# Performance work log

Hardware: AMD Instinct MI355X
Metric: run time of the kernel (lower is better)

Reference implementation:

```python
import jax, jax.numpy as jnp
import numpy as np

TAU = 0.2
LW = 0.5
EPS = 1e-12  # tf.math.l2_normalize epsilon


def _l2norm(x):
    ss = jnp.sum(x * x, axis=-1, keepdims=True)
    return x * jax.lax.rsqrt(jnp.maximum(ss, EPS))


def _global_head(f, W1, b1, W2, b2):
    g = jnp.mean(f, axis=(1, 2))            # GlobalAveragePooling2D -> [B, C]
    h = jax.nn.relu(g @ W1 + b1)
    return h @ W2 + b2                      # [B, 128]


def _dense_head(f, W1, b1, W2, b2):
    # 1x1 convs == per-pixel matmuls
    h = jax.nn.relu(jnp.einsum('bhwc,cd->bhwd', f, W1) + b1)
    return jnp.einsum('bhwd,de->bhwe', h, W2) + b2  # [B, H, W, 128]


def _info_nce(q, k):
    logits = (q @ k.T) / TAU                # [N, N]
    lse = jax.nn.logsumexp(logits, axis=-1)
    pos = jnp.diagonal(logits)
    return jnp.mean(lse - pos)


def setup_inputs() -> dict:
    key = jax.random.key(0)
    ks = jax.random.split(key, 10)
    B, H, W, C = 128, 7, 7, 2048
    Dh, De = 2048, 128
    s1 = 1.0 / np.sqrt(C)
    s2 = 1.0 / np.sqrt(Dh)
    inp = {
        'feat_q': jax.random.normal(ks[0], (B, H, W, C), jnp.float32),
        'feat_k': jax.random.normal(ks[1], (B, H, W, C), jnp.float32),
        'Wg1': jax.random.normal(ks[2], (C, Dh), jnp.float32) * s1,
        'bg1': jnp.zeros((Dh,), jnp.float32),
        'Wg2': jax.random.normal(ks[3], (Dh, De), jnp.float32) * s2,
        'bg2': jnp.zeros((De,), jnp.float32),
        'Wd1': jax.random.normal(ks[4], (C, Dh), jnp.float32) * s1,
        'bd1': jnp.zeros((Dh,), jnp.float32),
        'Wd2': jax.random.normal(ks[5], (Dh, De), jnp.float32) * s2,
        'bd2': jnp.zeros((De,), jnp.float32),
        'mWg1': jax.random.normal(ks[6], (C, Dh), jnp.float32) * s1,
        'mbg1': jnp.zeros((Dh,), jnp.float32),
        'mWg2': jax.random.normal(ks[7], (Dh, De), jnp.float32) * s2,
        'mbg2': jnp.zeros((De,), jnp.float32),
        'mWd1': jax.random.normal(ks[8], (C, Dh), jnp.float32) * s1,
        'mbd1': jnp.zeros((Dh,), jnp.float32),
        'mWd2': jax.random.normal(ks[9], (Dh, De), jnp.float32) * s2,
        'mbd2': jnp.zeros((De,), jnp.float32),
    }
    return inp


def reference(feat_q, feat_k, Wg1, bg1, Wg2, bg2, Wd1, bd1, Wd2, bd2,
              mWg1, mbg1, mWg2, mbg2, mWd1, mbd1, mWd2, mbd2):
    # query (student) branch
    q_g = _l2norm(_global_head(feat_q, Wg1, bg1, Wg2, bg2))      # [B, 128]
    q_d = _l2norm(_dense_head(feat_q, Wd1, bd1, Wd2, bd2))       # [B, H, W, 128]
    # key (momentum teacher) branch, stop-gradient as in train_step
    k_g = jax.lax.stop_gradient(_l2norm(_global_head(feat_k, mWg1, mbg1, mWg2, mbg2)))
    k_d = jax.lax.stop_gradient(_l2norm(_dense_head(feat_k, mWd1, mbd1, mWd2, mbd2)))

    l_g = _info_nce(q_g, k_g)

    B, H, W, De = q_d.shape
    f1 = q_d.reshape(B, H * W, De)
    f2 = k_d.reshape(B, H * W, De)
    sim = jnp.einsum('bnc,bmc->bnm', f1, f2)                     # [B, HW, HW]
    idx = jnp.argmax(sim, axis=-1)                               # [B, HW]
    matched = jnp.take_along_axis(f2, idx[..., None], axis=1)    # [B, HW, 128]

    l_d = _info_nce(f1.reshape(-1, De), matched.reshape(-1, De))
    total = (1.0 - LW) * l_g + LW * l_d
    return total
```

## Files before the change

kernel.cpp:

```cpp
#include <hip/hip_runtime.h>
#include <cstddef>

typedef __bf16 bf16x8 __attribute__((ext_vector_type(8)));
typedef float  f32x4  __attribute__((ext_vector_type(4)));
typedef unsigned short u16x8 __attribute__((ext_vector_type(8)));

__device__ __forceinline__ float b2f(unsigned short u) {
    union { unsigned int i; float f; } v; v.i = ((unsigned int)u) << 16; return v.f;
}
__device__ __forceinline__ unsigned short f2b(float f) {
    union { float f; unsigned int i; } v; v.f = f;
    unsigned int r = v.i + 0x7fffu + ((v.i >> 16) & 1u);
    return (unsigned short)(r >> 16);
}
__device__ __forceinline__ void gl_lds16(const void* g, void* l) {
    __builtin_amdgcn_global_load_lds((const __attribute__((address_space(1))) void*)g,
                                     (__attribute__((address_space(3))) void*)l,
                                     16, 0, 0);
}

__global__ __launch_bounds__(64) void detect_kernel(const unsigned short* __restrict__ feat,
                                                    int* __restrict__ flag) {
    __shared__ int cnt;
    if (threadIdx.x == 0) cnt = 0;
    __syncthreads();
    int c = 0;
    for (int i = threadIdx.x; i < 256; i += 64) {
        float v = b2f(feat[i]);
        if (fabsf(v) > 100.0f) ++c;
    }
    atomicAdd(&cnt, c);
    __syncthreads();
    if (threadIdx.x == 0) *flag = (cnt > 16) ? 1 : 0;
}

__global__ __launch_bounds__(256) void zero_kernel(float* __restrict__ p, int n4) {
    int i = blockIdx.x * 256 + threadIdx.x;
    const f32x4 z = {0.f, 0.f, 0.f, 0.f};
    if (i < n4) ((f32x4*)p)[i] = z;
}

__global__ __launch_bounds__(256) void pool_kernel(const void* __restrict__ fq,
                                                   const void* __restrict__ fk,
                                                   unsigned short* __restrict__ gq,
                                                   unsigned short* __restrict__ gk,
                                                   const int* __restrict__ flagp) {
    int fl = *flagp;
    int c = blockIdx.x * 256 + threadIdx.x;
    int b = blockIdx.y;
    const void* src = blockIdx.z ? fk : fq;
    unsigned short* dst = blockIdx.z ? gk : gq;
    size_t base = (size_t)b * 49 * 2048 + c;
    float s = 0.f;
    if (fl) {
        const float* sf = (const float*)src;
        #pragma unroll
        for (int p = 0; p < 49; ++p) s += sf[base + (size_t)p * 2048];
    } else {
        const unsigned short* su = (const unsigned short*)src;
        #pragma unroll
        for (int p = 0; p < 49; ++p) s += b2f(su[base + (size_t)p * 2048]);
    }
    dst[(size_t)b * 2048 + c] = f2b(s * (1.0f / 49.0f));
}

__global__ __launch_bounds__(256) void transpose4v_kernel(
    const void* __restrict__ s0, const void* __restrict__ s1,
    const void* __restrict__ s2, const void* __restrict__ s3,
    unsigned short* __restrict__ d0, unsigned short* __restrict__ d1,
    unsigned short* __restrict__ d2, unsigned short* __restrict__ d3,
    int rows, int cols, const int* __restrict__ flagp) {
    int fl = *flagp;
    int z = blockIdx.z;
    const void* in = (z == 0) ? s0 : (z == 1) ? s1 : (z == 2) ? s2 : s3;
    unsigned short* out = (z == 0) ? d0 : (z == 1) ? d1 : (z == 2) ? d2 : d3;
    __shared__ unsigned short tile[64 * 72];
    int bx = blockIdx.x * 64, by = blockIdx.y * 64;
    int tr = threadIdx.x >> 3;
    int tc = (threadIdx.x & 7) * 8;
    #pragma unroll
    for (int h = 0; h < 2; ++h) {
        int r = tr + h * 32;
        if (fl) {
            const float* inf = (const float*)in + (size_t)(by + r) * cols + bx + tc;
            f32x4 v0 = *(const f32x4*)inf;
            f32x4 v1 = *(const f32x4*)(inf + 4);
            u16x8 o;
            o[0]=f2b(v0[0]); o[1]=f2b(v0[1]); o[2]=f2b(v0[2]); o[3]=f2b(v0[3]);
            o[4]=f2b(v1[0]); o[5]=f2b(v1[1]); o[6]=f2b(v1[2]); o[7]=f2b(v1[3]);
            *(u16x8*)(tile + r * 72 + tc) = o;
        } else {
            const unsigned short* inu = (const unsigned short*)in + (size_t)(by + r) * cols + bx + tc;
            *(u16x8*)(tile + r * 72 + tc) = *(const u16x8*)inu;
        }
    }
    __syncthreads();
    #pragma unroll
    for (int h = 0; h < 2; ++h) {
        int oc = tr + h * 32;
        u16x8 v;
        #pragma unroll
        for (int j = 0; j < 8; ++j) v[j] = tile[(tc + j) * 72 + oc];
        *(u16x8*)(out + (size_t)(bx + oc) * rows + by + tc) = v;
    }
}

__global__ __launch_bounds__(256) void mlp_kernel(
    const void* __restrict__ Aq, const void* __restrict__ Ak,
    const unsigned short* __restrict__ gq, const unsigned short* __restrict__ gk,
    const unsigned short* __restrict__ BTdq, const unsigned short* __restrict__ BTdk,
    const unsigned short* __restrict__ BTgq, const unsigned short* __restrict__ BTgk,
    const unsigned short* __restrict__ W2dq, const unsigned short* __restrict__ W2dk,
    const unsigned short* __restrict__ W2gq, const unsigned short* __restrict__ W2gk,
    const void* __restrict__ b1dq, const void* __restrict__ b1dk,
    const void* __restrict__ b1gq, const void* __restrict__ b1gk,
    float* __restrict__ outdq, float* __restrict__ outdk,
    float* __restrict__ outgq, float* __restrict__ outgk,
    const int* __restrict__ flagp)
{
    int fl = *flagp;
    int z  = blockIdx.z;
    int isg = (blockIdx.y == 49);
    const void* A; const unsigned short* Bt; const unsigned short* W2;
    const void* b1; float* outp;
    if (!isg) {
        A = z ? Ak : Aq;  Bt = z ? BTdk : BTdq;  W2 = z ? W2dk : W2dq;
        b1 = z ? b1dk : b1dq;  outp = z ? outdk : outdq;
    } else {
        A = z ? (const void*)gk : (const void*)gq;  Bt = z ? BTgk : BTgq;
        W2 = z ? W2gk : W2gq;  b1 = z ? b1gk : b1gq;  outp = z ? outgk : outgq;
    }
    int af32 = (!isg) && fl;
    const int K = 2048;

    __shared__ unsigned short smem[8192 + 9216];
    unsigned short* As = smem;
    unsigned short* Bs = smem + 8192;
    unsigned short* Hs = smem + 8192;

    int tid  = threadIdx.x;
    int lane = tid & 63;
    int w    = tid >> 6;
    int wm = w & 1, wn = w >> 1;
    int quad = lane >> 4, l16 = lane & 15;
    size_t m0 = isg ? 0 : (size_t)blockIdx.y * 128;
    size_t n0 = (size_t)blockIdx.x * 128;

    int lrow = lane >> 3;
    int kc   = (lane & 7) ^ lrow;

    const unsigned short* gA[4];
    const unsigned short* gB[4];
    unsigned short* lA[4];
    unsigned short* lB[4];
    if (!af32) {
        const unsigned short* Au = (const unsigned short*)A;
        #pragma unroll
        for (int c = 0; c < 4; ++c) {
            int row = w * 32 + c * 8 + lrow;
            gA[c] = Au + (m0 + row) * (size_t)K + kc * 8;
            lA[c] = As + w * 2048 + c * 512;
        }
    }
    #pragma unroll
    for (int c = 0; c < 4; ++c) {
        int row = w * 32 + c * 8 + lrow;
        gB[c] = Bt + (n0 + row) * (size_t)K + kc * 8;
        lB[c] = Bs + w * 2048 + c * 512;
    }

    const f32x4 zero4 = {0.f, 0.f, 0.f, 0.f};
    f32x4 acc[4][4];
    #pragma unroll
    for (int i = 0; i < 4; ++i)
        #pragma unroll
        for (int j = 0; j < 4; ++j) acc[i][j] = zero4;

    int swz = l16 & 7;
    for (int kb = 0; kb < K / 64; ++kb) {
        __syncthreads();
        if (af32) {
            const float* Af = (const float*)A;
            #pragma unroll
            for (int i = 0; i < 4; ++i) {
                int l = tid + 256 * i;
                int row = l >> 3, kcp = l & 7;
                int kcg = kcp ^ (row & 7);
                size_t gidx = (m0 + row) * (size_t)K + kb * 64 + kcg * 8;
                f32x4 v0 = *(const f32x4*)(Af + gidx);
                f32x4 v1 = *(const f32x4*)(Af + gidx + 4);
                u16x8 o;
                o[0]=f2b(v0[0]); o[1]=f2b(v0[1]); o[2]=f2b(v0[2]); o[3]=f2b(v0[3]);
                o[4]=f2b(v1[0]); o[5]=f2b(v1[1]); o[6]=f2b(v1[2]); o[7]=f2b(v1[3]);
                *(u16x8*)(As + row * 64 + kcp * 8) = o;
            }
        } else {
            #pragma unroll
            for (int c = 0; c < 4; ++c) { gl_lds16(gA[c], lA[c]); gA[c] += 64; }
        }
        #pragma unroll
        for (int c = 0; c < 4; ++c) { gl_lds16(gB[c], lB[c]); gB[c] += 64; }
        __syncthreads();
        #pragma unroll
        for (int k0 = 0; k0 < 64; k0 += 32) {
            bf16x8 af[4], bfr[4];
            #pragma unroll
            for (int mt = 0; mt < 4; ++mt) {
                int row = wm * 64 + mt * 16 + l16;
                int sc  = (((k0 >> 3) + quad) ^ swz) << 3;
                af[mt] = *(const bf16x8*)(As + row * 64 + sc);
            }
            #pragma unroll
            for (int nt = 0; nt < 4; ++nt) {
                int row = wn * 64 + nt * 16 + l16;
                int sc  = (((k0 >> 3) + quad) ^ swz) << 3;
                bfr[nt] = *(const bf16x8*)(Bs + row * 64 + sc);
            }
            #pragma unroll
            for (int mt = 0; mt < 4; ++mt)
                #pragma unroll
                for (int nt = 0; nt < 4; ++nt)
                    acc[mt][nt] = __builtin_amdgcn_mfma_f32_16x16x32_bf16(af[mt], bfr[nt], acc[mt][nt], 0, 0, 0);
        }
    }

    float b1v[4];
    #pragma unroll
    for (int nt = 0; nt < 4; ++nt) {
        int col = (int)n0 + wn * 64 + nt * 16 + l16;
        b1v[nt] = fl ? ((const float*)b1)[col] : b2f(((const unsigned short*)b1)[col]);
    }

    f32x4 acc2[4][4];
    #pragma unroll
    for (int i = 0; i < 4; ++i)
        #pragma unroll
        for (int j = 0; j < 4; ++j) acc2[i][j] = zero4;

    #pragma unroll
    for (int hf = 0; hf < 2; ++hf) {
        __syncthreads();
        if (wn == hf) {
            #pragma unroll
            for (int mt = 0; mt < 4; ++mt)
                #pragma unroll
                for (int nt = 0; nt < 4; ++nt)
                    #pragma unroll
                    for (int r = 0; r < 4; ++r) {
                        float v = fmaxf(acc[mt][nt][r] + b1v[nt], 0.f);
                        Hs[(wm * 64 + mt * 16 + quad * 4 + r) * 72 + nt * 16 + l16] = f2b(v);
                    }
        } else {
            #pragma unroll
            for (int c = 0; c < 8; ++c) {
                const unsigned short* g = W2 + (size_t)(wm * 64 + c * 8 + lrow) * 2048
                                          + n0 + hf * 64 + kc * 8;
                gl_lds16(g, As + wm * 4096 + c * 512);
            }
        }
        __syncthreads();
        #pragma unroll
        for (int k0 = 0; k0 < 64; k0 += 32) {
            bf16x8 ha[4], wb[4];
            #pragma unroll
            for (int mt = 0; mt < 4; ++mt)
                ha[mt] = *(const bf16x8*)(Hs + (wm * 64 + mt * 16 + l16) * 72 + k0 + quad * 8);
            #pragma unroll
            for (int et = 0; et < 4; ++et) {
                int row = wn * 64 + et * 16 + l16;
                int sc  = (((k0 >> 3) + quad) ^ swz) << 3;
                wb[et] = *(const bf16x8*)(As + row * 64 + sc);
            }
            #pragma unroll
            for (int mt = 0; mt < 4; ++mt)
                #pragma unroll
                for (int et = 0; et < 4; ++et)
                    acc2[mt][et] = __builtin_amdgcn_mfma_f32_16x16x32_bf16(ha[mt], wb[et], acc2[mt][et], 0, 0, 0);
        }
    }

    #pragma unroll
    for (int et = 0; et < 4; ++et) {
        int col = wn * 64 + et * 16 + l16;
        #pragma unroll
        for (int mt = 0; mt < 4; ++mt)
            #pragma unroll
            for (int r = 0; r < 4; ++r) {
                size_t row = m0 + wm * 64 + mt * 16 + quad * 4 + r;
                atomicAdd(&outp[row * 128 + col], acc2[mt][et][r]);
            }
    }
}

__global__ __launch_bounds__(256) void simmatch_kernel(
    const float* __restrict__ rawdq, const float* __restrict__ rawdk,
    const void* __restrict__ bd2, const void* __restrict__ mbd2,
    unsigned short* __restrict__ qd, unsigned short* __restrict__ kd,
    unsigned short* __restrict__ matched, float* __restrict__ pos,
    const int* __restrict__ flagp) {
    int fl = *flagp;
    __shared__ float f1s[49 * 128];
    __shared__ float f2s[49 * 128];
    int b = blockIdx.x;
    int t = threadIdx.x;
    size_t base = (size_t)b * 49 * 128;

    int rr = t >> 2, jq = t & 3;
    if (rr < 49) {
        #pragma unroll
        for (int br = 0; br < 2; ++br) {
            const float* raw = br ? rawdk : rawdq;
            const void* bias = br ? mbd2 : bd2;
            unsigned short* outg = br ? kd : qd;
            float* fs = br ? f2s : f1s;
            size_t idx = base + (size_t)rr * 128 + jq * 32;
            float x[32];
            float ss = 0.f;
            #pragma unroll
            for (int c = 0; c < 32; ++c) {
                float bv = fl ? ((const float*)bias)[jq * 32 + c]
                              : b2f(((const unsigned short*)bias)[jq * 32 + c]);
                x[c] = raw[idx + c] + bv;
                ss += x[c] * x[c];
            }
            ss += __shfl_xor(ss, 1); ss += __shfl_xor(ss, 2);
            float rs = rsqrtf(fmaxf(ss, 1e-12f));
            #pragma unroll
            for (int c = 0; c < 32; ++c) {
                unsigned short us = f2b(x[c] * rs);
                outg[idx + c] = us;
                fs[rr * 128 + jq * 32 + c] = b2f(us);
            }
        }
    }
    __syncthreads();

    int i = t >> 2, q4 = t & 3;
    if (i < 49) {
        int mlo = q4 * 13;
        int mhi = mlo + 13; if (mhi > 49) mhi = 49;
        float best = -1e30f; int bi = 1 << 20;
        const f32x4* va = (const f32x4*)(f1s + i * 128);
        for (int m = mlo; m < mhi; ++m) {
            const f32x4* vb = (const f32x4*)(f2s + m * 128);
            float d = 0.f;
            #pragma unroll
            for (int j = 0; j < 32; ++j) {
                f32x4 a = va[j], bb = vb[j];
                d += a[0]*bb[0] + a[1]*bb[1] + a[2]*bb[2] + a[3]*bb[3];
            }
            if (d > best) { best = d; bi = m; }
        }
        #pragma unroll
        for (int off = 1; off < 4; off <<= 1) {
            float ov = __shfl_xor(best, off);
            int   oi = __shfl_xor(bi, off);
            if (ov > best || (ov == best && oi < bi)) { best = ov; bi = oi; }
        }
        if (q4 == 0) pos[b * 49 + i] = best * 5.0f;
        for (int j = q4 * 32; j < q4 * 32 + 32; ++j)
            matched[base + (size_t)i * 128 + j] = f2b(f2s[bi * 128 + j]);
    }
}

#define KS 136
__global__ __launch_bounds__(256) void lse_kernel(const unsigned short* __restrict__ qd,
                                                  const unsigned short* __restrict__ matched,
                                                  float* __restrict__ lsep) {
    __shared__ unsigned short As[128 * KS];
    __shared__ unsigned short Bs[64 * KS];
    __shared__ float rsum[128];
    int tid  = threadIdx.x;
    int lane = tid & 63, wave = tid >> 6;
    int wm = wave & 1, wn = wave >> 1;
    int quad = lane >> 4, l16 = lane & 15;
    size_t m0 = (size_t)blockIdx.x * 128;
    int z = blockIdx.y;

    #pragma unroll
    for (int i = 0; i < 8; ++i) {
        int l = tid + 256 * i;
        int row = l >> 4, ko = (l & 15) << 3;
        u16x8 v = *(const u16x8*)(qd + (m0 + row) * 128 + ko);
        *(u16x8*)(As + row * KS + ko) = v;
    }
    if (tid < 128) rsum[tid] = 0.f;

    float rs[4][4];
    #pragma unroll
    for (int mt = 0; mt < 4; ++mt)
        #pragma unroll
        for (int r = 0; r < 4; ++r) rs[mt][r] = 0.f;

    const f32x4 zero4 = {0.f, 0.f, 0.f, 0.f};
    int nlo = z * 448, nhi = nlo + 448;
    for (int n0 = nlo; n0 < nhi; n0 += 64) {
        __syncthreads();
        #pragma unroll
        for (int i = 0; i < 4; ++i) {
            int l = tid + 256 * i;
            int row = l >> 4, ko = (l & 15) << 3;
            u16x8 v = *(const u16x8*)(matched + (size_t)(n0 + row) * 128 + ko);
            *(u16x8*)(Bs + row * KS + ko) = v;
        }
        __syncthreads();
        f32x4 acc[4][2];
        #pragma unroll
        for (int mt = 0; mt < 4; ++mt) { acc[mt][0] = zero4; acc[mt][1] = zero4; }
        #pragma unroll
        for (int k0 = 0; k0 < 128; k0 += 32) {
            bf16x8 af[4], bfr[2];
            #pragma unroll
            for (int mt = 0; mt < 4; ++mt)
                af[mt] = *(const bf16x8*)(As + (wm * 64 + mt * 16 + l16) * KS + k0 + quad * 8);
            #pragma unroll
            for (int nt = 0; nt < 2; ++nt)
                bfr[nt] = *(const bf16x8*)(Bs + (wn * 32 + nt * 16 + l16) * KS + k0 + quad * 8);
            #pragma unroll
            for (int mt = 0; mt < 4; ++mt)
                #pragma unroll
                for (int nt = 0; nt < 2; ++nt)
                    acc[mt][nt] = __builtin_amdgcn_mfma_f32_16x16x32_bf16(af[mt], bfr[nt], acc[mt][nt], 0, 0, 0);
        }
        #pragma unroll
        for (int mt = 0; mt < 4; ++mt)
            #pragma unroll
            for (int r = 0; r < 4; ++r)
                rs[mt][r] += __expf(acc[mt][0][r] * 5.0f) + __expf(acc[mt][1][r] * 5.0f);
    }
    #pragma unroll
    for (int mt = 0; mt < 4; ++mt)
        #pragma unroll
        for (int r = 0; r < 4; ++r) {
            float v = rs[mt][r];
            v += __shfl_xor(v, 1); v += __shfl_xor(v, 2);
            v += __shfl_xor(v, 4); v += __shfl_xor(v, 8);
            if (l16 == 0) atomicAdd(&rsum[wm * 64 + mt * 16 + quad * 4 + r], v);
        }
    __syncthreads();
    if (tid < 128) lsep[(size_t)z * 6272 + m0 + tid] = rsum[tid];
}

__global__ __launch_bounds__(128) void lg_kernel(const float* __restrict__ rawgq,
                                                 const float* __restrict__ rawgk,
                                                 const void* __restrict__ bg2,
                                                 const void* __restrict__ mbg2,
                                                 float* __restrict__ lgrow,
                                                 const int* __restrict__ flagp) {
    int fl = *flagp;
    __shared__ float ksf[128 * 128];
    __shared__ float qsf[8 * 128];
    int t = threadIdx.x;
    int rbase = blockIdx.x * 8;
    {
        const float* rk = rawgk + (size_t)t * 128;
        float ss = 0.f;
        for (int c = 0; c < 128; ++c) {
            float bv = fl ? ((const float*)mbg2)[c] : b2f(((const unsigned short*)mbg2)[c]);
            float xx = rk[c] + bv;
            ss += xx * xx;
        }
        float rsv = rsqrtf(fmaxf(ss, 1e-12f));
        for (int c = 0; c < 128; ++c) {
            float bv = fl ? ((const float*)mbg2)[c] : b2f(((const unsigned short*)mbg2)[c]);
            ksf[t * 128 + c] = b2f(f2b((rk[c] + bv) * rsv));
        }
    }
    if (t < 8) {
        const float* rq = rawgq + (size_t)(rbase + t) * 128;
        float ss = 0.f;
        for (int c = 0; c < 128; ++c) {
            float bv = fl ? ((const float*)bg2)[c] : b2f(((const unsigned short*)bg2)[c]);
            float xx = rq[c] + bv;
            ss += xx * xx;
        }
        float rsv = rsqrtf(fmaxf(ss, 1e-12f));
        for (int c = 0; c < 128; ++c) {
            float bv = fl ? ((const float*)bg2)[c] : b2f(((const unsigned short*)bg2)[c]);
            qsf[t * 128 + c] = b2f(f2b((rq[c] + bv) * rsv));
        }
    }
    __syncthreads();
    int rl = t >> 4, jg = t & 15;
    int row = rbase + rl;
    float se = 0.f, diag = 0.f;
    for (int jj = 0; jj < 8; ++jj) {
        int j = jg * 8 + jj;
        float d = 0.f;
        #pragma unroll 8
        for (int c = 0; c < 128; ++c) d += qsf[rl * 128 + c] * ksf[j * 128 + c];
        d *= 5.0f;
        se += __expf(d);
        if (j == row) diag = d;
    }
    #pragma unroll
    for (int off = 1; off < 16; off <<= 1) { se += __shfl_xor(se, off); diag += __shfl_xor(diag, off); }
    if (jg == 0) lgrow[row] = logf(se) - diag;
}

__global__ __launch_bounds__(256) void final_kernel(const float* __restrict__ lsep,
                                                    const float* __restrict__ pos,
                                                    const float* __restrict__ lgrow,
                                                    unsigned int* __restrict__ out) {
    int t = threadIdx.x;
    float s = 0.f;
    for (int i = t; i < 6272; i += 256) {
        float se = 0.f;
        #pragma unroll
        for (int zz = 0; zz < 14; ++zz) se += lsep[zz * 6272 + i];
        s += logf(se) - pos[i];
    }
    float g = (t < 128) ? lgrow[t] : 0.f;
    #pragma unroll
    for (int off = 32; off >= 1; off >>= 1) { s += __shfl_xor(s, off); g += __shfl_xor(g, off); }
    __shared__ float p8[8];
    if ((t & 63) == 0) { p8[t >> 6] = s; p8[4 + (t >> 6)] = g; }
    __syncthreads();
    if (t == 0) {
        float ld  = (p8[0] + p8[1] + p8[2] + p8[3]) * (1.0f / 6272.0f);
        float lg  = (p8[4] + p8[5] + p8[6] + p8[7]) * (1.0f / 128.0f);
        float total = 0.5f * lg + 0.5f * ld;
        unsigned int L = f2b(total);
        union { float f; unsigned int u; } tb; tb.f = total;
        unsigned int base = (tb.u & 0xFFFF0000u) | L;
        unsigned int bu = base; float be = 1e30f;
        #pragma unroll
        for (int d = -1; d <= 1; ++d) {
            unsigned int c = base + ((unsigned int)d << 16);
            union { unsigned int u; float f; } cv; cv.u = c;
            float e = fabsf(cv.f - total);
            if (e < be) { be = e; bu = c; }
        }
        out[0] = bu;
    }
}

#define BT1Q_OFF  ((size_t)0)
#define QD_OFF    ((size_t)0)
#define KD_OFF    ((size_t)1605632)
#define MT_OFF    ((size_t)3211264)
#define BT1K_OFF  ((size_t)8388608)
#define BTGQ_OFF  ((size_t)16777216)
#define BTGK_OFF  ((size_t)25165824)
#define W2DQ_OFF  ((size_t)33554432)
#define W2DK_OFF  ((size_t)34078720)
#define W2GQ_OFF  ((size_t)34603008)
#define W2GK_OFF  ((size_t)35127296)
#define RAWDQ_OFF ((size_t)35651584)
#define RAWDK_OFF ((size_t)38862848)
#define RAWGQ_OFF ((size_t)42074112)
#define RAWGK_OFF ((size_t)42139648)
#define GQ_OFF    ((size_t)42205184)
#define GK_OFF    ((size_t)42729472)
#define POS_OFF   ((size_t)43253760)
#define LSEP_OFF  ((size_t)43278848)
#define LGR_OFF   ((size_t)43630080)
#define FLAG_OFF  ((size_t)43630592)

extern "C" void kernel_launch(void* const* d_in, const int* in_sizes, int n_in,
                              void* d_out, int out_size, void* d_ws, size_t ws_size,
                              hipStream_t stream) {
    (void)in_sizes; (void)n_in; (void)out_size; (void)ws_size;
    const void* feat_q = d_in[0];
    const void* feat_k = d_in[1];
    const void* Wg1 = d_in[2];  const void* bg1 = d_in[3];
    const void* Wg2 = d_in[4];  const void* bg2 = d_in[5];
    const void* Wd1 = d_in[6];  const void* bd1 = d_in[7];
    const void* Wd2 = d_in[8];  const void* bd2 = d_in[9];
    const void* mWg1 = d_in[10]; const void* mbg1 = d_in[11];
    const void* mWg2 = d_in[12]; const void* mbg2 = d_in[13];
    const void* mWd1 = d_in[14]; const void* mbd1 = d_in[15];
    const void* mWd2 = d_in[16]; const void* mbd2 = d_in[17];

    char* ws = (char*)d_ws;
    unsigned short* BT1q = (unsigned short*)(ws + BT1Q_OFF);
    unsigned short* BT1k = (unsigned short*)(ws + BT1K_OFF);
    unsigned short* BTgq = (unsigned short*)(ws + BTGQ_OFF);
    unsigned short* BTgk = (unsigned short*)(ws + BTGK_OFF);
    unsigned short* W2dq = (unsigned short*)(ws + W2DQ_OFF);
    unsigned short* W2dk = (unsigned short*)(ws + W2DK_OFF);
    unsigned short* W2gq = (unsigned short*)(ws + W2GQ_OFF);
    unsigned short* W2gk = (unsigned short*)(ws + W2GK_OFF);
    float* rawdq = (float*)(ws + RAWDQ_OFF);
    float* rawdk = (float*)(ws + RAWDK_OFF);
    float* rawgq = (float*)(ws + RAWGQ_OFF);
    float* rawgk = (float*)(ws + RAWGK_OFF);
    unsigned short* gq = (unsigned short*)(ws + GQ_OFF);
    unsigned short* gk = (unsigned short*)(ws + GK_OFF);
    unsigned short* qd = (unsigned short*)(ws + QD_OFF);
    unsigned short* kd = (unsigned short*)(ws + KD_OFF);
    unsigned short* mt = (unsigned short*)(ws + MT_OFF);
    float* pos  = (float*)(ws + POS_OFF);
    float* lsep = (float*)(ws + LSEP_OFF);
    float* lgr  = (float*)(ws + LGR_OFF);
    int*   flag = (int*)(ws + FLAG_OFF);

    detect_kernel<<<1, 64, 0, stream>>>((const unsigned short*)feat_q, flag);

    transpose4v_kernel<<<dim3(32, 32, 4), 256, 0, stream>>>(
        Wd1, mWd1, Wg1, mWg1, BT1q, BT1k, BTgq, BTgk, 2048, 2048, flag);
    transpose4v_kernel<<<dim3(2, 32, 4), 256, 0, stream>>>(
        Wd2, mWd2, Wg2, mWg2, W2dq, W2dk, W2gq, W2gk, 2048, 128, flag);

    pool_kernel<<<dim3(8, 128, 2), 256, 0, stream>>>(feat_q, feat_k, gq, gk, flag);

    zero_kernel<<<1600, 256, 0, stream>>>(rawdq, 409600);

    mlp_kernel<<<dim3(16, 50, 2), 256, 0, stream>>>(
        feat_q, feat_k, gq, gk,
        BT1q, BT1k, BTgq, BTgk,
        W2dq, W2dk, W2gq, W2gk,
        bd1, mbd1, bg1, mbg1,
        rawdq, rawdk, rawgq, rawgk, flag);

    simmatch_kernel<<<128, 256, 0, stream>>>(rawdq, rawdk, bd2, mbd2, qd, kd, mt, pos, flag);
    lse_kernel<<<dim3(49, 14), 256, 0, stream>>>(qd, mt, lsep);
    lg_kernel<<<16, 128, 0, stream>>>(rawgq, rawgk, bg2, mbg2, lgr, flag);
    final_kernel<<<1, 256, 0, stream>>>(lsep, pos, lgr, (unsigned int*)d_out);
}
```

Measured before the change: 641.4 us.

## Pre-convert features to bf16 and split MLP into sequential passes with reused buffers

Fp32 features are converted to bf16 in a separate pass, so the MLP GEMM always uses direct global-to-LDS loads instead of converting inline. The single fused launch covering global and dense, query and key, becomes sequential launches that reuse two workspace slots, which shrinks the working set and may improve L2 residency. The LSE split count drops from 14 to 7 to halve partial results. The cost is more launches, an extra read and write of each feature tensor, and less parallelism per launch.

```diff
diff --git a/kernel.cpp b/kernel.cpp
--- a/kernel.cpp
+++ b/kernel.cpp
@@ -38,6 +38,24 @@
     int i = blockIdx.x * 256 + threadIdx.x;
     const f32x4 z = {0.f, 0.f, 0.f, 0.f};
     if (i < n4) ((f32x4*)p)[i] = z;
+}
+
+__global__ __launch_bounds__(256) void convert_kernel(const void* __restrict__ in,
+                                                      unsigned short* __restrict__ out,
+                                                      const int* __restrict__ flagp) {
+    int fl = *flagp;
+    size_t i = ((size_t)blockIdx.x * 256 + threadIdx.x) * 8;
+    if (fl) {
+        const float* inf = (const float*)in;
+        f32x4 v0 = *(const f32x4*)(inf + i);
+        f32x4 v1 = *(const f32x4*)(inf + i + 4);
+        u16x8 o;
+        o[0]=f2b(v0[0]); o[1]=f2b(v0[1]); o[2]=f2b(v0[2]); o[3]=f2b(v0[3]);
+        o[4]=f2b(v1[0]); o[5]=f2b(v1[1]); o[6]=f2b(v1[2]); o[7]=f2b(v1[3]);
+        *(u16x8*)(out + i) = o;
+    } else {
+        *(u16x8*)(out + i) = *(const u16x8*)((const unsigned short*)in + i);
+    }
 }
 
 __global__ __launch_bounds__(256) void pool_kernel(const void* __restrict__ fq,
@@ -64,6 +82,45 @@
     dst[(size_t)b * 2048 + c] = f2b(s * (1.0f / 49.0f));
 }
 
+__global__ __launch_bounds__(256) void transpose2v_kernel(
+    const void* __restrict__ s0, const void* __restrict__ s1,
+    unsigned short* __restrict__ d0, unsigned short* __restrict__ d1,
+    int rows, int cols, const int* __restrict__ flagp) {
+    int fl = *flagp;
+    int z = blockIdx.z;
+    const void* in = z ? s1 : s0;
+    unsigned short* out = z ? d1 : d0;
+    __shared__ unsigned short tile[64 * 72];
+    int bx = blockIdx.x * 64, by = blockIdx.y * 64;
+    int tr = threadIdx.x >> 3;
+    int tc = (threadIdx.x & 7) * 8;
+    #pragma unroll
+    for (int h = 0; h < 2; ++h) {
+        int r = tr + h * 32;
+        if (fl) {
+            const float* inf = (const float*)in + (size_t)(by + r) * cols + bx + tc;
+            f32x4 v0 = *(const f32x4*)inf;
+            f32x4 v1 = *(const f32x4*)(inf + 4);
+            u16x8 o;
+            o[0]=f2b(v0[0]); o[1]=f2b(v0[1]); o[2]=f2b(v0[2]); o[3]=f2b(v0[3]);
+            o[4]=f2b(v1[0]); o[5]=f2b(v1[1]); o[6]=f2b(v1[2]); o[7]=f2b(v1[3]);
+            *(u16x8*)(tile + r * 72 + tc) = o;
+        } else {
+            const unsigned short* inu = (const unsigned short*)in + (size_t)(by + r) * cols + bx + tc;
+            *(u16x8*)(tile + r * 72 + tc) = *(const u16x8*)inu;
+        }
+    }
+    __syncthreads();
+    #pragma unroll
+    for (int h = 0; h < 2; ++h) {
+        int oc = tr + h * 32;
+        u16x8 v;
+        #pragma unroll
+        for (int j = 0; j < 8; ++j) v[j] = tile[(tc + j) * 72 + oc];
+        *(u16x8*)(out + (size_t)(bx + oc) * rows + by + tc) = v;
+    }
+}
+
 __global__ __launch_bounds__(256) void transpose4v_kernel(
     const void* __restrict__ s0, const void* __restrict__ s1,
     const void* __restrict__ s2, const void* __restrict__ s3,
@@ -106,31 +163,20 @@
 }
 
 __global__ __launch_bounds__(256) void mlp_kernel(
-    const void* __restrict__ Aq, const void* __restrict__ Ak,
-    const unsigned short* __restrict__ gq, const unsigned short* __restrict__ gk,
-    const unsigned short* __restrict__ BTdq, const unsigned short* __restrict__ BTdk,
-    const unsigned short* __restrict__ BTgq, const unsigned short* __restrict__ BTgk,
-    const unsigned short* __restrict__ W2dq, const unsigned short* __restrict__ W2dk,
-    const unsigned short* __restrict__ W2gq, const unsigned short* __restrict__ W2gk,
-    const void* __restrict__ b1dq, const void* __restrict__ b1dk,
-    const void* __restrict__ b1gq, const void* __restrict__ b1gk,
-    float* __restrict__ outdq, float* __restrict__ outdk,
-    float* __restrict__ outgq, float* __restrict__ outgk,
+    const unsigned short* __restrict__ A0, const unsigned short* __restrict__ A1,
+    const unsigned short* __restrict__ Bt0, const unsigned short* __restrict__ Bt1,
+    const unsigned short* __restrict__ W20, const unsigned short* __restrict__ W21,
+    const void* __restrict__ b10, const void* __restrict__ b11,
+    float* __restrict__ out0, float* __restrict__ out1,
     const int* __restrict__ flagp)
 {
     int fl = *flagp;
     int z  = blockIdx.z;
-    int isg = (blockIdx.y == 49);
-    const void* A; const unsigned short* Bt; const unsigned short* W2;
-    const void* b1; float* outp;
-    if (!isg) {
-        A = z ? Ak : Aq;  Bt = z ? BTdk : BTdq;  W2 = z ? W2dk : W2dq;
-        b1 = z ? b1dk : b1dq;  outp = z ? outdk : outdq;
-    } else {
-        A = z ? (const void*)gk : (const void*)gq;  Bt = z ? BTgk : BTgq;
-        W2 = z ? W2gk : W2gq;  b1 = z ? b1gk : b1gq;  outp = z ? outgk : outgq;
-    }
-    int af32 = (!isg) && fl;
+    const unsigned short* A  = z ? A1 : A0;
+    const unsigned short* Bt = z ? Bt1 : Bt0;
+    const unsigned short* W2 = z ? W21 : W20;
+    const void* b1 = z ? b11 : b10;
+    float* outp = z ? out1 : out0;
     const int K = 2048;
 
     __shared__ unsigned short smem[8192 + 9216];
@@ -143,7 +189,7 @@
     int w    = tid >> 6;
     int wm = w & 1, wn = w >> 1;
     int quad = lane >> 4, l16 = lane & 15;
-    size_t m0 = isg ? 0 : (size_t)blockIdx.y * 128;
+    size_t m0 = (size_t)blockIdx.y * 128;
     size_t n0 = (size_t)blockIdx.x * 128;
 
     int lrow = lane >> 3;
@@ -153,19 +199,12 @@
     const unsigned short* gB[4];
     unsigned short* lA[4];
     unsigned short* lB[4];
-    if (!af32) {
-        const unsigned short* Au = (const unsigned short*)A;
-        #pragma unroll
-        for (int c = 0; c < 4; ++c) {
-            int row = w * 32 + c * 8 + lrow;
-            gA[c] = Au + (m0 + row) * (size_t)K + kc * 8;
-            lA[c] = As + w * 2048 + c * 512;
-        }
-    }
     #pragma unroll
     for (int c = 0; c < 4; ++c) {
         int row = w * 32 + c * 8 + lrow;
+        gA[c] = A  + (m0 + row) * (size_t)K + kc * 8;
         gB[c] = Bt + (n0 + row) * (size_t)K + kc * 8;
+        lA[c] = As + w * 2048 + c * 512;
         lB[c] = Bs + w * 2048 + c * 512;
     }
 
@@ -179,25 +218,8 @@
     int swz = l16 & 7;
     for (int kb = 0; kb < K / 64; ++kb) {
         __syncthreads();
-        if (af32) {
-            const float* Af = (const float*)A;
-            #pragma unroll
-            for (int i = 0; i < 4; ++i) {
-                int l = tid + 256 * i;
-                int row = l >> 3, kcp = l & 7;
-                int kcg = kcp ^ (row & 7);
-                size_t gidx = (m0 + row) * (size_t)K + kb * 64 + kcg * 8;
-                f32x4 v0 = *(const f32x4*)(Af + gidx);
-                f32x4 v1 = *(const f32x4*)(Af + gidx + 4);
-                u16x8 o;
-                o[0]=f2b(v0[0]); o[1]=f2b(v0[1]); o[2]=f2b(v0[2]); o[3]=f2b(v0[3]);
-                o[4]=f2b(v1[0]); o[5]=f2b(v1[1]); o[6]=f2b(v1[2]); o[7]=f2b(v1[3]);
-                *(u16x8*)(As + row * 64 + kcp * 8) = o;
-            }
-        } else {
-            #pragma unroll
-            for (int c = 0; c < 4; ++c) { gl_lds16(gA[c], lA[c]); gA[c] += 64; }
-        }
+        #pragma unroll
+        for (int c = 0; c < 4; ++c) { gl_lds16(gA[c], lA[c]); gA[c] += 64; }
         #pragma unroll
         for (int c = 0; c < 4; ++c) { gl_lds16(gB[c], lB[c]); gB[c] += 64; }
         __syncthreads();
@@ -393,7 +415,7 @@
         for (int r = 0; r < 4; ++r) rs[mt][r] = 0.f;
 
     const f32x4 zero4 = {0.f, 0.f, 0.f, 0.f};
-    int nlo = z * 448, nhi = nlo + 448;
+    int nlo = z * 896, nhi = nlo + 896;
     for (int n0 = nlo; n0 < nhi; n0 += 64) {
         __syncthreads();
         #pragma unroll
@@ -507,7 +529,7 @@
     for (int i = t; i < 6272; i += 256) {
         float se = 0.f;
         #pragma unroll
-        for (int zz = 0; zz < 14; ++zz) se += lsep[zz * 6272 + i];
+        for (int zz = 0; zz < 7; ++zz) se += lsep[zz * 6272 + i];
         s += logf(se) - pos[i];
     }
     float g = (t < 128) ? lgrow[t] : 0.f;
@@ -535,27 +557,25 @@
     }
 }
 
-#define BT1Q_OFF  ((size_t)0)
+#define SLOTA_OFF ((size_t)0)
 #define QD_OFF    ((size_t)0)
 #define KD_OFF    ((size_t)1605632)
 #define MT_OFF    ((size_t)3211264)
-#define BT1K_OFF  ((size_t)8388608)
-#define BTGQ_OFF  ((size_t)16777216)
-#define BTGK_OFF  ((size_t)25165824)
-#define W2DQ_OFF  ((size_t)33554432)
-#define W2DK_OFF  ((size_t)34078720)
-#define W2GQ_OFF  ((size_t)34603008)
-#define W2GK_OFF  ((size_t)35127296)
-#define RAWDQ_OFF ((size_t)35651584)
-#define RAWDK_OFF ((size_t)38862848)
-#define RAWGQ_OFF ((size_t)42074112)
-#define RAWGK_OFF ((size_t)42139648)
-#define GQ_OFF    ((size_t)42205184)
-#define GK_OFF    ((size_t)42729472)
-#define POS_OFF   ((size_t)43253760)
-#define LSEP_OFF  ((size_t)43278848)
-#define LGR_OFF   ((size_t)43630080)
-#define FLAG_OFF  ((size_t)43630592)
+#define SLOTB_OFF ((size_t)8388608)
+#define W2DQ_OFF  ((size_t)34078720)
+#define W2DK_OFF  ((size_t)34603008)
+#define W2GQ_OFF  ((size_t)35127296)
+#define W2GK_OFF  ((size_t)35651584)
+#define RAWDQ_OFF ((size_t)36175872)
+#define RAWDK_OFF ((size_t)39387136)
+#define RAWGQ_OFF ((size_t)42598400)
+#define RAWGK_OFF ((size_t)42663936)
+#define GQ_OFF    ((size_t)42729472)
+#define GK_OFF    ((size_t)43253760)
+#define POS_OFF   ((size_t)42729472)
+#define LSEP_OFF  ((size_t)42754560)
+#define LGR_OFF   ((size_t)42930176)
+#define FLAG_OFF  ((size_t)42930688)
 
 extern "C" void kernel_launch(void* const* d_in, const int* in_sizes, int n_in,
                               void* d_out, int out_size, void* d_ws, size_t ws_size,
@@ -573,10 +593,8 @@
     const void* mWd2 = d_in[16]; const void* mbd2 = d_in[17];
 
     char* ws = (char*)d_ws;
-    unsigned short* BT1q = (unsigned short*)(ws + BT1Q_OFF);
-    unsigned short* BT1k = (unsigned short*)(ws + BT1K_OFF);
-    unsigned short* BTgq = (unsigned short*)(ws + BTGQ_OFF);
-    unsigned short* BTgk = (unsigned short*)(ws + BTGK_OFF);
+    unsigned short* slotA = (unsigned short*)(ws + SLOTA_OFF);
+    unsigned short* slotB = (unsigned short*)(ws + SLOTB_OFF);
     unsigned short* W2dq = (unsigned short*)(ws + W2DQ_OFF);
     unsigned short* W2dk = (unsigned short*)(ws + W2DK_OFF);
     unsigned short* W2gq = (unsigned short*)(ws + W2GQ_OFF);
@@ -597,24 +615,29 @@
 
     detect_kernel<<<1, 64, 0, stream>>>((const unsigned short*)feat_q, flag);
 
-    transpose4v_kernel<<<dim3(32, 32, 4), 256, 0, stream>>>(
-        Wd1, mWd1, Wg1, mWg1, BT1q, BT1k, BTgq, BTgk, 2048, 2048, flag);
+    pool_kernel<<<dim3(8, 128, 2), 256, 0, stream>>>(feat_q, feat_k, gq, gk, flag);
+
+    transpose2v_kernel<<<dim3(32, 32, 2), 256, 0, stream>>>(Wg1, mWg1, slotA, slotB, 2048, 2048, flag);
     transpose4v_kernel<<<dim3(2, 32, 4), 256, 0, stream>>>(
         Wd2, mWd2, Wg2, mWg2, W2dq, W2dk, W2gq, W2gk, 2048, 128, flag);
 
-    pool_kernel<<<dim3(8, 128, 2), 256, 0, stream>>>(feat_q, feat_k, gq, gk, flag);
-
     zero_kernel<<<1600, 256, 0, stream>>>(rawdq, 409600);
 
-    mlp_kernel<<<dim3(16, 50, 2), 256, 0, stream>>>(
-        feat_q, feat_k, gq, gk,
-        BT1q, BT1k, BTgq, BTgk,
-        W2dq, W2dk, W2gq, W2gk,
-        bd1, mbd1, bg1, mbg1,
-        rawdq, rawdk, rawgq, rawgk, flag);
+    mlp_kernel<<<dim3(16, 1, 2), 256, 0, stream>>>(
+        gq, gk, slotA, slotB, W2gq, W2gk, bg1, mbg1, rawgq, rawgk, flag);
+
+    transpose2v_kernel<<<dim3(32, 32, 1), 256, 0, stream>>>(Wd1, Wd1, slotA, slotA, 2048, 2048, flag);
+    convert_kernel<<<6272, 256, 0, stream>>>(feat_q, slotB, flag);
+    mlp_kernel<<<dim3(16, 49, 1), 256, 0, stream>>>(
+        slotB, slotB, slotA, slotA, W2dq, W2dq, bd1, bd1, rawdq, rawdq, flag);
+
+    transpose2v_kernel<<<dim3(32, 32, 1), 256, 0, stream>>>(mWd1, mWd1, slotA, slotA, 2048, 2048, flag);
+    convert_kernel<<<6272, 256, 0, stream>>>(feat_k, slotB, flag);
+    mlp_kernel<<<dim3(16, 49, 1), 256, 0, stream>>>(
+        slotB, slotB, slotA, slotA, W2dk, W2dk, mbd1, mbd1, rawdk, rawdk, flag);
 
     simmatch_kernel<<<128, 256, 0, stream>>>(rawdq, rawdk, bd2, mbd2, qd, kd, mt, pos, flag);
-    lse_kernel<<<dim3(49, 14), 256, 0, stream>>>(qd, mt, lsep);
+    lse_kernel<<<dim3(49, 7), 256, 0, stream>>>(qd, mt, lsep);
     lg_kernel<<<16, 128, 0, stream>>>(rawgq, rawgk, bg2, mbg2, lgr, flag);
     final_kernel<<<1, 256, 0, stream>>>(lsep, pos, lgr, (unsigned int*)d_out);
 }
```

Result: no change. 636.6 us (-0.7%).
